# Performance work log

Hardware: AMD Instinct MI355X
Metric: run time of the kernel (lower is better)

## Reference

```python
import jax, jax.numpy as jnp
import numpy as np

B, S, D, H = 2, 2048, 2048, 16
HD = D // H
RESIDUAL_SCALE = 1.0
EPS = 1e-6


def setup_inputs() -> dict:
    key = jax.random.key(0)
    ks = jax.random.split(key, 6)
    x = jax.random.normal(ks[0], (B, S, D), jnp.float32)
    # rotary tables: emb = cat(freqs, freqs), shape [S, HD]
    inv_freq = 1.0 / (10000.0 ** (jnp.arange(0, HD, 2, dtype=jnp.float32) / HD))
    t = jnp.arange(S, dtype=jnp.float32)
    freqs = jnp.einsum('s,f->sf', t, inv_freq)
    emb = jnp.concatenate([freqs, freqs], axis=-1)
    cos, sin = jnp.cos(emb), jnp.sin(emb)
    sc = 0.02
    w_qkv = jax.random.normal(ks[1], (3 * D, D), jnp.float32) * sc
    w_out = jax.random.normal(ks[2], (D, D), jnp.float32) * sc
    w_fc1 = jax.random.normal(ks[3], (4 * D, D), jnp.float32) * sc
    w_fc2 = jax.random.normal(ks[4], (D, 4 * D), jnp.float32) * sc
    g1 = jnp.ones((D,), jnp.float32)
    g2 = jnp.ones((D,), jnp.float32)
    return {'x': x, 'cos': cos, 'sin': sin, 'g1': g1, 'g2': g2,
            'w_qkv': w_qkv, 'w_out': w_out, 'w_fc1': w_fc1, 'w_fc2': w_fc2}


def _rmsnorm(x, g):
    xf = x.astype(jnp.float32)
    norm = jnp.sqrt(jnp.mean(xf * xf, axis=-1, keepdims=True) + EPS)
    return g * (xf / norm)


def _rotate_half(x):
    x1, x2 = jnp.split(x, 2, axis=-1)
    return jnp.concatenate([-x2, x1], axis=-1)


def _rope(t, cos, sin):
    # t: [B, S, H, HD]; cos/sin: [S, HD]
    c = cos[None, :, None, :]
    s = sin[None, :, None, :]
    return t * c + _rotate_half(t) * s


def reference(x, cos, sin, g1, g2, w_qkv, w_out, w_fc1, w_fc2):
    b, s, d = x.shape
    x_skip = x
    h = _rmsnorm(x, g1)
    qkv = (h @ w_qkv.T).reshape(b, s, 3, H, HD)
    q = _rope(qkv[:, :, 0], cos, sin)
    k = _rope(qkv[:, :, 1], cos, sin)
    v = qkv[:, :, 2]  # rotary is identity on v
    scale = 1.0 / jnp.sqrt(jnp.asarray(HD, dtype=q.dtype))
    scores = jnp.einsum('bqhd,bkhd->bhqk', q, k) * scale
    causal = jnp.triu(jnp.ones((s, s), dtype=bool), k=1)
    scores = jnp.where(causal[None, None], -jnp.inf, scores)
    attn = jax.nn.softmax(scores, axis=-1)
    o = jnp.einsum('bhqk,bkhd->bqhd', attn, v).reshape(b, s, d)
    x = x_skip + RESIDUAL_SCALE * (o @ w_out.T)
    x_skip = x
    h = _rmsnorm(x, g2)
    h = jax.nn.gelu(h @ w_fc1.T, approximate=True) @ w_fc2.T
    return x_skip + RESIDUAL_SCALE * h
```

## Files before the change

kernel.cpp:

```cpp
#include <hip/hip_runtime.h>
#include <stdint.h>

typedef unsigned short u16;
typedef u16 u16x4 __attribute__((ext_vector_type(4)));
typedef u16 u16x8 __attribute__((ext_vector_type(8)));
typedef __bf16 bf16x8 __attribute__((ext_vector_type(8)));
typedef float f32x4 __attribute__((ext_vector_type(4)));
typedef float f32x16 __attribute__((ext_vector_type(16)));

#define MFMA16 __builtin_amdgcn_mfma_f32_16x16x32_bf16
#define MFMA32 __builtin_amdgcn_mfma_f32_32x32x16_bf16

static __device__ __forceinline__ float b2f(u16 u) {
    union { unsigned int i; float f; } v; v.i = ((unsigned int)u) << 16; return v.f;
}
static __device__ __forceinline__ u16 f2b(float f) {
    union { float f; unsigned int i; } v; v.f = f;
    unsigned int r = (v.i + 0x7fffu + ((v.i >> 16) & 1u)) >> 16;
    return (u16)r;
}
static __device__ __forceinline__ unsigned pk2(float lo, float hi) {
    union { __bf16 b[2]; unsigned u; } t;
    t.b[0] = (__bf16)lo; t.b[1] = (__bf16)hi; return t.u;
}
static __device__ __forceinline__ void gload_lds16(const void* g, void* l) {
    __builtin_amdgcn_global_load_lds((__attribute__((address_space(1))) void*)g,
                                     (__attribute__((address_space(3))) void*)l,
                                     16, 0, 0);
}

__global__ __launch_bounds__(256) void cvt_k(const float* __restrict__ in,
                                             u16* __restrict__ out, long n) {
    long i = ((long)blockIdx.x * 256 + threadIdx.x) * 4;
    if (i >= n) return;
    float4 v = *(const float4*)(in + i);
    u16x4 o; o[0] = f2b(v.x); o[1] = f2b(v.y); o[2] = f2b(v.z); o[3] = f2b(v.w);
    *(u16x4*)(out + i) = o;
}

__global__ __launch_bounds__(256) void addred_k(float* __restrict__ xout,
                                                const float* __restrict__ p0,
                                                const float* __restrict__ p1) {
    long i = ((long)blockIdx.x * 256 + threadIdx.x) * 4;
    float4 a = *(const float4*)(xout + i);
    float4 b = *(const float4*)(p0 + i);
    float4 c = *(const float4*)(p1 + i);
    a.x += b.x + c.x; a.y += b.y + c.y; a.z += b.z + c.z; a.w += b.w + c.w;
    *(float4*)(xout + i) = a;
}

__global__ __launch_bounds__(256) void addrednorm_k(float* __restrict__ xout,
                                                    const float* __restrict__ x,
                                                    const float* __restrict__ p0,
                                                    const float* __restrict__ p1,
                                                    const float* __restrict__ g,
                                                    u16* __restrict__ out) {
    const long row = blockIdx.x;
    const int tid = threadIdx.x;
    const long base = row * 2048;
    float4 a = *(const float4*)(x + base + tid * 4);
    float4 b = *(const float4*)(p0 + base + tid * 4);
    float4 c = *(const float4*)(p1 + base + tid * 4);
    a.x += b.x + c.x; a.y += b.y + c.y; a.z += b.z + c.z; a.w += b.w + c.w;
    float4 a2 = *(const float4*)(x + base + 1024 + tid * 4);
    float4 b2 = *(const float4*)(p0 + base + 1024 + tid * 4);
    float4 c2 = *(const float4*)(p1 + base + 1024 + tid * 4);
    a2.x += b2.x + c2.x; a2.y += b2.y + c2.y;
    a2.z += b2.z + c2.z; a2.w += b2.w + c2.w;
    *(float4*)(xout + base + tid * 4) = a;
    *(float4*)(xout + base + 1024 + tid * 4) = a2;
    float ss = a.x*a.x + a.y*a.y + a.z*a.z + a.w*a.w
             + a2.x*a2.x + a2.y*a2.y + a2.z*a2.z + a2.w*a2.w;
    #pragma unroll
    for (int d = 1; d < 64; d <<= 1) ss += __shfl_xor(ss, d);
    __shared__ float red[4];
    if ((tid & 63) == 0) red[tid >> 6] = ss;
    __syncthreads();
    float tot = red[0] + red[1] + red[2] + red[3];
    float rinv = rsqrtf(tot * (1.0f / 2048.0f) + 1e-6f);
    float4 g0 = *(const float4*)(g + tid * 4);
    float4 g1 = *(const float4*)(g + 1024 + tid * 4);
    u16x4 o0, o1;
    o0[0] = f2b(a.x * g0.x * rinv); o0[1] = f2b(a.y * g0.y * rinv);
    o0[2] = f2b(a.z * g0.z * rinv); o0[3] = f2b(a.w * g0.w * rinv);
    o1[0] = f2b(a2.x * g1.x * rinv); o1[1] = f2b(a2.y * g1.y * rinv);
    o1[2] = f2b(a2.z * g1.z * rinv); o1[3] = f2b(a2.w * g1.w * rinv);
    *(u16x4*)(out + base + tid * 4) = o0;
    *(u16x4*)(out + base + 1024 + tid * 4) = o1;
}

__global__ __launch_bounds__(256) void rmsnorm_k(const float* __restrict__ x,
                                                 const float* __restrict__ g,
                                                 u16* __restrict__ out) {
    const long row = blockIdx.x;
    const int tid = threadIdx.x;
    const float* xr = x + row * 2048;
    float4 a = *(const float4*)(xr + tid * 4);
    float4 b = *(const float4*)(xr + 1024 + tid * 4);
    float ss = a.x*a.x + a.y*a.y + a.z*a.z + a.w*a.w
             + b.x*b.x + b.y*b.y + b.z*b.z + b.w*b.w;
    #pragma unroll
    for (int d = 1; d < 64; d <<= 1) ss += __shfl_xor(ss, d);
    __shared__ float red[4];
    if ((tid & 63) == 0) red[tid >> 6] = ss;
    __syncthreads();
    float tot = red[0] + red[1] + red[2] + red[3];
    float rinv = rsqrtf(tot * (1.0f / 2048.0f) + 1e-6f);
    float4 g0 = *(const float4*)(g + tid * 4);
    float4 g1 = *(const float4*)(g + 1024 + tid * 4);
    u16x4 o0, o1;
    o0[0] = f2b(a.x * g0.x * rinv); o0[1] = f2b(a.y * g0.y * rinv);
    o0[2] = f2b(a.z * g0.z * rinv); o0[3] = f2b(a.w * g0.w * rinv);
    o1[0] = f2b(b.x * g1.x * rinv); o1[1] = f2b(b.y * g1.y * rinv);
    o1[2] = f2b(b.z * g1.z * rinv); o1[3] = f2b(b.w * g1.w * rinv);
    *(u16x4*)(out + row * 2048 + tid * 4) = o0;
    *(u16x4*)(out + row * 2048 + 1024 + tid * 4) = o1;
}

__global__ __launch_bounds__(256) void rope_k(u16* __restrict__ qkv,
                                              const float* __restrict__ cosb,
                                              const float* __restrict__ sinb) {
    long idx = (long)blockIdx.x * 256 + threadIdx.x;
    int d = (int)(idx & 15) * 4;
    int h = (int)((idx >> 4) & 15);
    int which = (int)((idx >> 8) & 1);
    long row = idx >> 9;
    int s = (int)(row & 2047);
    u16* base = qkv + row * 6144 + which * 2048 + h * 128;
    u16x4 ua = *(u16x4*)(base + d);
    u16x4 ub = *(u16x4*)(base + d + 64);
    float4 c4 = *(const float4*)(cosb + (long)s * 128 + d);
    float4 s4 = *(const float4*)(sinb + (long)s * 128 + d);
    float cc[4] = {c4.x, c4.y, c4.z, c4.w};
    float sn[4] = {s4.x, s4.y, s4.z, s4.w};
    float scale = (which == 0) ? 0.08838834764831845f : 1.0f;
    u16x4 oa, ob;
    #pragma unroll
    for (int j = 0; j < 4; ++j) {
        float a = b2f(ua[j]), b = b2f(ub[j]);
        oa[j] = f2b((a * cc[j] - b * sn[j]) * scale);
        ob[j] = f2b((b * cc[j] + a * sn[j]) * scale);
    }
    *(u16x4*)(base + d) = oa;
    *(u16x4*)(base + d + 64) = ob;
}

__global__ __launch_bounds__(256) void vtrans_k(const u16* __restrict__ qkv,
                                                u16* __restrict__ vt) {
    __shared__ u16 t[128 * 65];
    const int bh = blockIdx.y, b = bh >> 4, h = bh & 15;
    const int s0 = blockIdx.x * 64;
    const int tid = threadIdx.x;
    #pragma unroll
    for (int it = 0; it < 4; ++it) {
        int flat = it * 256 + tid;
        int sl = flat >> 4, slot = flat & 15;
        u16x8 v = *(const u16x8*)(qkv + (long)(b * 2048 + s0 + sl) * 6144 + 4096 +
                                  h * 128 + slot * 8);
        #pragma unroll
        for (int j = 0; j < 8; ++j) t[(slot * 8 + j) * 65 + sl] = v[j];
    }
    __syncthreads();
    #pragma unroll
    for (int it = 0; it < 4; ++it) {
        int flat = it * 256 + tid;
        int d = flat >> 3, sg = flat & 7;
        u16x8 v;
        #pragma unroll
        for (int j = 0; j < 8; ++j) v[j] = t[d * 65 + sg * 8 + j];
        *(u16x8*)(vt + ((long)bh * 128 + d) * 2048 + s0 + sg * 8) = v;
    }
}

#define DS_A(BUF, SM, KK) (*(const bf16x8*)(ldsb + (BUF)*32768 + \
        ((((SM)*2) + (KK)) << 10) + rin64 + cst2))
#define DS_B(BUF, SN, KK) (*(const bf16x8*)(ldsb + 65536 + (BUF)*32768 + \
        ((((SN)*2) + (KK)) << 10) + rin64 + cst2))
#define STAGE_A(BUF, SK, KT) do { \
    gload_lds16(sA0 + ((long)(KT)*64 + (SK)*32), ldsb + (BUF)*32768 + (w4 + (SK))*1024); \
    gload_lds16(sA1 + ((long)(KT)*64 + (SK)*32), ldsb + (BUF)*32768 + (w4 + 2 + (SK))*1024); \
} while (0)
#define STAGE_B(BUF, SK, KT) do { \
    gload_lds16(sB0 + ((long)(KT)*64 + (SK)*32), ldsb + 65536 + (BUF)*32768 + (w4 + (SK))*1024); \
    gload_lds16(sB1 + ((long)(KT)*64 + (SK)*32), ldsb + 65536 + (BUF)*32768 + (w4 + 2 + (SK))*1024); \
} while (0)
#define PHASE(BUF, MH, KK, RDB, STAGE_STMT, VM) do { \
    bf16x8 af[4]; \
    _Pragma("unroll") \
    for (int m = 0; m < 4; ++m) af[m] = DS_A(BUF, wr8 + (MH)*4 + m, KK); \
    if (RDB) { \
        bfr[0] = DS_B(BUF, wc4 + 0, KK); bfr[1] = DS_B(BUF, wc4 + 1, KK); \
        bfr[2] = DS_B(BUF, wc4 + 2, KK); bfr[3] = DS_B(BUF, wc4 + 3, KK); \
    } \
    STAGE_STMT; \
    if (VM) { asm volatile("s_waitcnt vmcnt(6)" ::: "memory"); } \
    __builtin_amdgcn_sched_barrier(0); \
    __builtin_amdgcn_s_barrier(); \
    __builtin_amdgcn_sched_barrier(0); \
    __builtin_amdgcn_s_setprio(1); \
    _Pragma("unroll") \
    for (int m = 0; m < 4; ++m) \
        _Pragma("unroll") \
        for (int n = 0; n < 4; ++n) \
            acc[(MH)*4 + m][n] = MFMA16(af[m], bfr[n], acc[(MH)*4 + m][n], 0, 0, 0); \
    __builtin_amdgcn_s_setprio(0); \
    __builtin_amdgcn_sched_barrier(0); \
    __builtin_amdgcn_s_barrier(); \
    __builtin_amdgcn_sched_barrier(0); \
} while (0)

template <int EPI>
__global__ __launch_bounds__(512, 2) void gemm256(const u16* __restrict__ A,
                                                  const u16* __restrict__ W,
                                                  int M, int N, int K,
                                                  u16* outb, float* outf,
                                                  const float* res, int ksplit) {
    __shared__ u16 lds_[65536];
    char* ldsb = (char*)lds_;
    const int tid = threadIdx.x;
    const int w = tid >> 6, l = tid & 63;
    const int w4 = w * 4;
    const int wr8 = (w >> 2) * 8;
    const int wc4 = (w & 3) * 4;
    const int rin64 = (l & 15) * 64;
    const int cst2 = ((((l >> 4) * 8) ^ (((l >> 3) & 1) << 4)) << 1);

    const int nbn = N >> 8;
    const int nbm = M >> 8;
    const int nwg = gridDim.x;
    const int cpx = nwg >> 3;
    const int bid = blockIdx.x;
    int wg = (bid & 7) * cpx + (bid >> 3);
    int kseg = 0;
    int Keff = K;
    if (ksplit == 2) {
        kseg = wg & 1;
        wg >>= 1;
        Keff = K >> 1;
    }
    const int grp = 8 * nbn;
    const int g8 = wg / grp;
    const int rem = wg - g8 * grp;
    const int bm0 = g8 * 8;
    const int gmh = (nbm - bm0 < 8) ? (nbm - bm0) : 8;
    const int bn = rem / gmh;
    const int bm = bm0 + rem % gmh;
    const u16* Ab = A + (long)kseg * Keff;
    const u16* Wb = W + (long)kseg * Keff;

    const int r4 = l >> 2;
    const int clog = ((l & 3) * 8) ^ (((r4 >> 3) & 1) << 4);
    const u16* sA0 = Ab + ((long)bm * 256 + (w * 2 + 0) * 16 + r4) * K + clog;
    const u16* sA1 = Ab + ((long)bm * 256 + (w * 2 + 1) * 16 + r4) * K + clog;
    const u16* sB0 = Wb + ((long)bn * 256 + (w * 2 + 0) * 16 + r4) * K + clog;
    const u16* sB1 = Wb + ((long)bn * 256 + (w * 2 + 1) * 16 + r4) * K + clog;

    f32x4 acc[8][4];
    #pragma unroll
    for (int m = 0; m < 8; ++m)
        #pragma unroll
        for (int n = 0; n < 4; ++n) acc[m][n] = (f32x4){0.f, 0.f, 0.f, 0.f};
    bf16x8 bfr[4];

    const int nkt = Keff >> 6;
    const int niter = nkt >> 1;

    STAGE_B(0, 0, 0); STAGE_A(0, 0, 0); STAGE_B(0, 1, 0); STAGE_A(0, 1, 0);
    STAGE_B(1, 0, 1); STAGE_A(1, 0, 1); STAGE_B(1, 1, 1);
    asm volatile("s_waitcnt vmcnt(6)" ::: "memory");
    __builtin_amdgcn_sched_barrier(0);
    __builtin_amdgcn_s_barrier();
    __builtin_amdgcn_sched_barrier(0);

    for (int it = 0; it < niter; ++it) {
        const int t = it * 2;
        const int t1 = t + 1;
        const int t2 = (t + 2 < nkt) ? t + 2 : nkt - 1;
        const int t3 = (t + 3 < nkt) ? t + 3 : nkt - 1;
        PHASE(0, 0, 0, 1, STAGE_A(1, 1, t1), 0);
        PHASE(0, 1, 0, 0, STAGE_B(0, 0, t2), 0);
        PHASE(0, 0, 1, 1, STAGE_A(0, 0, t2), 0);
        PHASE(0, 1, 1, 0, STAGE_B(0, 1, t2), 1);
        PHASE(1, 0, 0, 1, STAGE_A(0, 1, t2), 0);
        PHASE(1, 1, 0, 0, STAGE_B(1, 0, t3), 0);
        PHASE(1, 0, 1, 1, STAGE_A(1, 0, t3), 0);
        PHASE(1, 1, 1, 0, STAGE_B(1, 1, t3), 1);
    }
    asm volatile("s_waitcnt vmcnt(0)" ::: "memory");

    const int rb = bm * 256 + (wr8 >> 3) * 128 + ((l >> 4) << 2);
    const int cb = bn * 256 + (w & 3) * 64 + (l & 15);
    float* pf = (EPI == 3) ? (outf + (long)kseg * M * N) : outf;
    #pragma unroll
    for (int m = 0; m < 8; ++m) {
        #pragma unroll
        for (int r = 0; r < 4; ++r) {
            long row = rb + m * 16 + r;
            #pragma unroll
            for (int n = 0; n < 4; ++n) {
                long col = cb + n * 16;
                float v = acc[m][n][r];
                if (EPI == 1) {
                    pf[row * N + col] = res[row * N + col] + v;
                } else if (EPI == 2) {
                    float u = 0.7978845608028654f * v * (1.0f + 0.044715f * v * v);
                    float e = __expf(2.0f * u);
                    float tgl = 1.0f - 2.0f / (e + 1.0f);
                    outb[row * N + col] = f2b(0.5f * v * (1.0f + tgl));
                } else if (EPI == 3) {
                    pf[row * N + col] = v;
                } else {
                    outb[row * N + col] = f2b(v);
                }
            }
        }
    }
}

struct AttnState {
    f32x16 acc[4];
    float m_i, l_i;
};

template <bool DIAG>
static __device__ __forceinline__ void attn_tile(
    int kv0, int qg, bool do_g1, int l31, int hi,
    const u16* __restrict__ Ks, const u16* __restrict__ Vt,
    const bf16x8 (&qf)[8], AttnState& st)
{
    f32x16 sacc0, sacc1;
    #pragma unroll
    for (int r = 0; r < 16; ++r) { sacc0[r] = 0.f; sacc1[r] = 0.f; }

    #pragma unroll
    for (int dsl = 0; dsl < 8; ++dsl) {
        int slot = dsl * 2 + hi;
        int kv = l31;
        int sw = (slot & 8) | ((slot & 7) ^ (kv & 7));
        bf16x8 kf = *(const bf16x8*)(Ks + kv * 128 + sw * 8);
        sacc0 = MFMA32(kf, qf[dsl], sacc0, 0, 0, 0);
    }
    if (do_g1) {
        #pragma unroll
        for (int dsl = 0; dsl < 8; ++dsl) {
            int slot = dsl * 2 + hi;
            int kv = 32 + l31;
            int sw = (slot & 8) | ((slot & 7) ^ (kv & 7));
            bf16x8 kf = *(const bf16x8*)(Ks + kv * 128 + sw * 8);
            sacc1 = MFMA32(kf, qf[dsl], sacc1, 0, 0, 0);
        }
    }

    float sv[2][16];
    #pragma unroll
    for (int r = 0; r < 16; ++r) {
        sv[0][r] = sacc0[r];
        sv[1][r] = do_g1 ? sacc1[r] : -INFINITY;
    }
    if (DIAG) {
        #pragma unroll
        for (int g = 0; g < 2; ++g)
            #pragma unroll
            for (int r = 0; r < 16; ++r) {
                int kvg = kv0 + g * 32 + ((r & 3) + 8 * (r >> 2) + 4 * hi);
                if (kvg > qg) sv[g][r] = -INFINITY;
            }
    }

    float mx = sv[0][0];
    #pragma unroll
    for (int r = 1; r < 16; ++r) mx = fmaxf(mx, sv[0][r]);
    #pragma unroll
    for (int r = 0; r < 16; ++r) mx = fmaxf(mx, sv[1][r]);
    mx = fmaxf(mx, __shfl_xor(mx, 32));

    bool defer = __all(mx <= st.m_i + 8.0f);
    if (!defer) {
        float mnew = fmaxf(st.m_i, mx);
        float f = __expf(st.m_i - mnew);
        st.l_i *= f;
        #pragma unroll
        for (int dblk = 0; dblk < 4; ++dblk)
            #pragma unroll
            for (int r = 0; r < 16; ++r) st.acc[dblk][r] *= f;
        st.m_i = mnew;
    }

    float ssum = 0.f;
    #pragma unroll
    for (int g = 0; g < 2; ++g)
        #pragma unroll
        for (int r = 0; r < 16; ++r) {
            float e = __expf(sv[g][r] - st.m_i);
            sv[g][r] = e;
            ssum += e;
        }
    ssum += __shfl_xor(ssum, 32);
    st.l_i += ssum;

    unsigned w[2][4][2];
    #pragma unroll
    for (int g = 0; g < 2; ++g)
        #pragma unroll
        for (int q4 = 0; q4 < 4; ++q4) {
            w[g][q4][0] = pk2(sv[g][4 * q4 + 0], sv[g][4 * q4 + 1]);
            w[g][q4][1] = pk2(sv[g][4 * q4 + 2], sv[g][4 * q4 + 3]);
        }
    bf16x8 pfrag[4];
    #pragma unroll
    for (int ks = 0; ks < 4; ++ks) {
        int g = ks >> 1, h2 = ks & 1;
        unsigned o0 = hi ? w[g][2 * h2 + 1][0] : w[g][2 * h2][0];
        unsigned o1 = hi ? w[g][2 * h2 + 1][1] : w[g][2 * h2][1];
        unsigned t0 = hi ? w[g][2 * h2][0] : w[g][2 * h2 + 1][0];
        unsigned t1 = hi ? w[g][2 * h2][1] : w[g][2 * h2 + 1][1];
        unsigned s0v = __shfl_xor(t0, 32);
        unsigned s1v = __shfl_xor(t1, 32);
        union { unsigned u[4]; bf16x8 v; } cv;
        cv.u[0] = hi ? s0v : o0;
        cv.u[1] = hi ? s1v : o1;
        cv.u[2] = hi ? o0 : s0v;
        cv.u[3] = hi ? o1 : s1v;
        pfrag[ks] = cv.v;
    }

    #pragma unroll
    for (int dblk = 0; dblk < 4; ++dblk) {
        int d = dblk * 32 + l31;
        #pragma unroll
        for (int ks = 0; ks < 4; ++ks) {
            if (ks >= 2 && !do_g1) continue;
            int slot = ks * 2 + hi;
            bf16x8 vf = *(const bf16x8*)(Vt + d * 64 + (slot ^ (d & 7)) * 8);
            st.acc[dblk] = MFMA32(vf, pfrag[ks], st.acc[dblk], 0, 0, 0);
        }
    }
}

__global__ __launch_bounds__(256) void attn3_k(const u16* __restrict__ qkv,
                                               const u16* __restrict__ vt,
                                               u16* __restrict__ out) {
    const int bh = blockIdx.y;
    const int b = bh >> 4, h = bh & 15;
    const int qb = blockIdx.x;
    const int q0 = qb * 128;
    const int tid = threadIdx.x, wave = tid >> 6, lane = tid & 63;
    const int l31 = lane & 31, hi = lane >> 5;
    const int brow = b * 2048;
    __shared__ u16 Ks_lds[2][64 * 128];
    __shared__ u16 Vt_lds[2][128 * 64];

    const int krow = tid >> 4;
    const int kslot = tid & 15;
    const int vrow = tid >> 3;
    const int vslot = tid & 7;

    bf16x8 qf[8];
    {
        const u16* qp = qkv + (long)(brow + q0 + wave * 32 + l31) * 6144 +
                        h * 128 + hi * 8;
        #pragma unroll
        for (int dsl = 0; dsl < 8; ++dsl) qf[dsl] = *(const bf16x8*)(qp + dsl * 16);
    }

    AttnState st;
    st.m_i = -INFINITY; st.l_i = 0.f;
    #pragma unroll
    for (int dblk = 0; dblk < 4; ++dblk)
        #pragma unroll
        for (int r = 0; r < 16; ++r) st.acc[dblk][r] = 0.f;

    const int r0 = q0 + wave * 32;
    const int qg = r0 + l31;
    const int nt = 2 * qb + 2;
    int cur = 0;

#define STAGE_KV(BUF, KV0) do { \
    _Pragma("unroll") \
    for (int i = 0; i < 4; ++i) { \
        int kv = i * 16 + krow; \
        int sw = (kslot & 8) | ((kslot & 7) ^ (kv & 7)); \
        const u16* src = qkv + (long)(brow + (KV0) + kv) * 6144 + 2048 + \
                         h * 128 + sw * 8; \
        gload_lds16(src, (char*)Ks_lds[BUF] + (i * 16 + wave * 4) * 256); \
    } \
    _Pragma("unroll") \
    for (int i = 0; i < 4; ++i) { \
        int d = i * 32 + vrow; \
        int sw = vslot ^ (d & 7); \
        const u16* src = vt + ((long)bh * 128 + d) * 2048 + (KV0) + sw * 8; \
        gload_lds16(src, (char*)Vt_lds[BUF] + (i * 32 + wave * 8) * 128); \
    } \
} while (0)

    STAGE_KV(0, 0);
    for (int t = 0; t < nt; ++t) {
        const int kv0 = t * 64;
        const bool more = (t + 1 < nt);
        if (more) {
            if (cur) STAGE_KV(0, kv0 + 64); else STAGE_KV(1, kv0 + 64);
        }
        if (more) { asm volatile("s_waitcnt vmcnt(8)" ::: "memory"); }
        else      { asm volatile("s_waitcnt vmcnt(0)" ::: "memory"); }
        __builtin_amdgcn_sched_barrier(0);
        __builtin_amdgcn_s_barrier();
        __builtin_amdgcn_sched_barrier(0);
        {
            const u16* Ks = Ks_lds[cur];
            const u16* Vt_ = Vt_lds[cur];
            const int delta = r0 - kv0;
            if (delta >= 64)
                attn_tile<false>(kv0, qg, true, l31, hi, Ks, Vt_, qf, st);
            else if (delta >= 0)
                attn_tile<true>(kv0, qg, delta >= 32, l31, hi, Ks, Vt_, qf, st);
        }
        __builtin_amdgcn_sched_barrier(0);
        __builtin_amdgcn_s_barrier();
        __builtin_amdgcn_sched_barrier(0);
        cur ^= 1;
    }
#undef STAGE_KV

    float inv = 1.0f / st.l_i;
    long orow = (long)(brow + q0 + wave * 32 + l31);
    #pragma unroll
    for (int dblk = 0; dblk < 4; ++dblk)
        #pragma unroll
        for (int rq = 0; rq < 4; ++rq) {
            u16x4 o4;
            #pragma unroll
            for (int m = 0; m < 4; ++m) o4[m] = f2b(st.acc[dblk][rq * 4 + m] * inv);
            int d = dblk * 32 + 8 * rq + 4 * hi;
            *(u16x4*)(out + orow * 2048 + h * 128 + d) = o4;
        }
}

extern "C" void kernel_launch(void* const* d_in, const int* in_sizes, int n_in,
                              void* d_out, int out_size, void* d_ws, size_t ws_size,
                              hipStream_t stream) {
    const float* x     = (const float*)d_in[0];
    const float* cosb  = (const float*)d_in[1];
    const float* sinb  = (const float*)d_in[2];
    const float* g1    = (const float*)d_in[3];
    const float* g2    = (const float*)d_in[4];
    const float* w_qkv = (const float*)d_in[5];
    const float* w_out = (const float*)d_in[6];
    const float* w_fc1 = (const float*)d_in[7];
    const float* w_fc2 = (const float*)d_in[8];

    char* ws = (char*)d_ws;
    u16* wqkv_b = (u16*)(ws);
    u16* wout_b = (u16*)(ws + 25165824);
    u16* wfc1_b = (u16*)(ws + 33554432);
    u16* wfc2_b = (u16*)(ws + 67108864);
    u16* h_b    = (u16*)(ws + 100663296);
    u16* qkv_b  = (u16*)(ws + 117440512);
    u16* attn_b = (u16*)(ws + 167772160);
    u16* vt_b   = h_b;
    u16* hg_b   = qkv_b;
    float* part = (float*)ws;
    float* pop  = (float*)(ws + 100663296);
    float* xout = (float*)d_out;

    cvt_k<<<12288, 256, 0, stream>>>(w_qkv, wqkv_b, 12582912L);
    cvt_k<<<4096, 256, 0, stream>>>(w_out, wout_b, 4194304L);
    cvt_k<<<16384, 256, 0, stream>>>(w_fc1, wfc1_b, 16777216L);
    cvt_k<<<16384, 256, 0, stream>>>(w_fc2, wfc2_b, 16777216L);

    rmsnorm_k<<<4096, 256, 0, stream>>>(x, g1, h_b);
    gemm256<0><<<384, 512, 0, stream>>>(h_b, wqkv_b, 4096, 6144, 2048,
                                        qkv_b, nullptr, nullptr, 1);
    rope_k<<<8192, 256, 0, stream>>>(qkv_b, cosb, sinb);
    vtrans_k<<<dim3(32, 32), 256, 0, stream>>>(qkv_b, vt_b);
    attn3_k<<<dim3(16, 32), 256, 0, stream>>>(qkv_b, vt_b, attn_b);
    gemm256<3><<<256, 512, 0, stream>>>(attn_b, wout_b, 4096, 2048, 2048,
                                        nullptr, pop, nullptr, 2);
    addrednorm_k<<<4096, 256, 0, stream>>>(xout, x, pop, pop + 8388608, g2, h_b);
    gemm256<2><<<512, 512, 0, stream>>>(h_b, wfc1_b, 4096, 8192, 2048,
                                        hg_b, nullptr, nullptr, 1);
    gemm256<3><<<256, 512, 0, stream>>>(hg_b, wfc2_b, 4096, 2048, 8192,
                                        nullptr, part, nullptr, 2);
    addred_k<<<8192, 256, 0, stream>>>(xout, part, part + 8388608);
}
```

Measured before the change: 604.7 us.

## Fuse V transpose into QKV GEMM epilogue and merge A/B staging

The QKV projection GEMM gets a new epilogue that writes the V columns directly in transposed [b,h,d,s] layout into the output buffer. This removes the separate vtrans kernel and its extra read and write of V. The GEMM main loop now issues A and B tile loads together in every other phase rather than alternating them, with the vmcnt wait adjusted to match. Workspace aliasing is also rearranged so the out-projection partial sums land in d_out and the qkv region, which drops __restrict__ on addrednorm because its output now aliases an input. The V epilogue writes short strided u16x4 stores, and the staging change alters how memory loads overlap with the MFMA work.

```diff
diff --git a/kernel.cpp b/kernel.cpp
--- a/kernel.cpp
+++ b/kernel.cpp
@@ -49,9 +49,9 @@
     *(float4*)(xout + i) = a;
 }
 
-__global__ __launch_bounds__(256) void addrednorm_k(float* __restrict__ xout,
+__global__ __launch_bounds__(256) void addrednorm_k(float* xout,
                                                     const float* __restrict__ x,
-                                                    const float* __restrict__ p0,
+                                                    const float* p0,
                                                     const float* __restrict__ p1,
                                                     const float* __restrict__ g,
                                                     u16* __restrict__ out) {
@@ -145,42 +145,13 @@
     *(u16x4*)(base + d + 64) = ob;
 }
 
-__global__ __launch_bounds__(256) void vtrans_k(const u16* __restrict__ qkv,
-                                                u16* __restrict__ vt) {
-    __shared__ u16 t[128 * 65];
-    const int bh = blockIdx.y, b = bh >> 4, h = bh & 15;
-    const int s0 = blockIdx.x * 64;
-    const int tid = threadIdx.x;
-    #pragma unroll
-    for (int it = 0; it < 4; ++it) {
-        int flat = it * 256 + tid;
-        int sl = flat >> 4, slot = flat & 15;
-        u16x8 v = *(const u16x8*)(qkv + (long)(b * 2048 + s0 + sl) * 6144 + 4096 +
-                                  h * 128 + slot * 8);
-        #pragma unroll
-        for (int j = 0; j < 8; ++j) t[(slot * 8 + j) * 65 + sl] = v[j];
-    }
-    __syncthreads();
-    #pragma unroll
-    for (int it = 0; it < 4; ++it) {
-        int flat = it * 256 + tid;
-        int d = flat >> 3, sg = flat & 7;
-        u16x8 v;
-        #pragma unroll
-        for (int j = 0; j < 8; ++j) v[j] = t[d * 65 + sg * 8 + j];
-        *(u16x8*)(vt + ((long)bh * 128 + d) * 2048 + s0 + sg * 8) = v;
-    }
-}
-
 #define DS_A(BUF, SM, KK) (*(const bf16x8*)(ldsb + (BUF)*32768 + \
         ((((SM)*2) + (KK)) << 10) + rin64 + cst2))
 #define DS_B(BUF, SN, KK) (*(const bf16x8*)(ldsb + 65536 + (BUF)*32768 + \
         ((((SN)*2) + (KK)) << 10) + rin64 + cst2))
-#define STAGE_A(BUF, SK, KT) do { \
+#define STAGE_AB(BUF, SK, KT) do { \
     gload_lds16(sA0 + ((long)(KT)*64 + (SK)*32), ldsb + (BUF)*32768 + (w4 + (SK))*1024); \
     gload_lds16(sA1 + ((long)(KT)*64 + (SK)*32), ldsb + (BUF)*32768 + (w4 + 2 + (SK))*1024); \
-} while (0)
-#define STAGE_B(BUF, SK, KT) do { \
     gload_lds16(sB0 + ((long)(KT)*64 + (SK)*32), ldsb + 65536 + (BUF)*32768 + (w4 + (SK))*1024); \
     gload_lds16(sB1 + ((long)(KT)*64 + (SK)*32), ldsb + 65536 + (BUF)*32768 + (w4 + 2 + (SK))*1024); \
 } while (0)
@@ -193,7 +164,7 @@
         bfr[2] = DS_B(BUF, wc4 + 2, KK); bfr[3] = DS_B(BUF, wc4 + 3, KK); \
     } \
     STAGE_STMT; \
-    if (VM) { asm volatile("s_waitcnt vmcnt(6)" ::: "memory"); } \
+    if (VM) { asm volatile("s_waitcnt vmcnt(8)" ::: "memory"); } \
     __builtin_amdgcn_sched_barrier(0); \
     __builtin_amdgcn_s_barrier(); \
     __builtin_amdgcn_sched_barrier(0); \
@@ -214,7 +185,8 @@
                                                   const u16* __restrict__ W,
                                                   int M, int N, int K,
                                                   u16* outb, float* outf,
-                                                  const float* res, int ksplit) {
+                                                  float* outf2, const float* res,
+                                                  u16* vtw, int ksplit) {
     __shared__ u16 lds_[65536];
     char* ldsb = (char*)lds_;
     const int tid = threadIdx.x;
@@ -265,9 +237,8 @@
     const int nkt = Keff >> 6;
     const int niter = nkt >> 1;
 
-    STAGE_B(0, 0, 0); STAGE_A(0, 0, 0); STAGE_B(0, 1, 0); STAGE_A(0, 1, 0);
-    STAGE_B(1, 0, 1); STAGE_A(1, 0, 1); STAGE_B(1, 1, 1);
-    asm volatile("s_waitcnt vmcnt(6)" ::: "memory");
+    STAGE_AB(0, 0, 0); STAGE_AB(0, 1, 0); STAGE_AB(1, 0, 1);
+    asm volatile("s_waitcnt vmcnt(8)" ::: "memory");
     __builtin_amdgcn_sched_barrier(0);
     __builtin_amdgcn_s_barrier();
     __builtin_amdgcn_sched_barrier(0);
@@ -277,20 +248,46 @@
         const int t1 = t + 1;
         const int t2 = (t + 2 < nkt) ? t + 2 : nkt - 1;
         const int t3 = (t + 3 < nkt) ? t + 3 : nkt - 1;
-        PHASE(0, 0, 0, 1, STAGE_A(1, 1, t1), 0);
-        PHASE(0, 1, 0, 0, STAGE_B(0, 0, t2), 0);
-        PHASE(0, 0, 1, 1, STAGE_A(0, 0, t2), 0);
-        PHASE(0, 1, 1, 0, STAGE_B(0, 1, t2), 1);
-        PHASE(1, 0, 0, 1, STAGE_A(0, 1, t2), 0);
-        PHASE(1, 1, 0, 0, STAGE_B(1, 0, t3), 0);
-        PHASE(1, 0, 1, 1, STAGE_A(1, 0, t3), 0);
-        PHASE(1, 1, 1, 0, STAGE_B(1, 1, t3), 1);
+        PHASE(0, 0, 0, 1, STAGE_AB(1, 1, t1), 0);
+        PHASE(0, 1, 0, 0, ;, 1);
+        PHASE(0, 0, 1, 1, STAGE_AB(0, 0, t2), 0);
+        PHASE(0, 1, 1, 0, ;, 1);
+        PHASE(1, 0, 0, 1, STAGE_AB(0, 1, t2), 0);
+        PHASE(1, 1, 0, 0, ;, 1);
+        PHASE(1, 0, 1, 1, STAGE_AB(1, 0, t3), 0);
+        PHASE(1, 1, 1, 0, ;, 1);
     }
     asm volatile("s_waitcnt vmcnt(0)" ::: "memory");
 
     const int rb = bm * 256 + (wr8 >> 3) * 128 + ((l >> 4) << 2);
     const int cb = bn * 256 + (w & 3) * 64 + (l & 15);
-    float* pf = (EPI == 3) ? (outf + (long)kseg * M * N) : outf;
+    if (EPI == 4) {
+        const bool vreg = (cb >= 4096);
+        #pragma unroll
+        for (int m = 0; m < 8; ++m) {
+            long row0 = rb + m * 16;
+            #pragma unroll
+            for (int n = 0; n < 4; ++n) {
+                long col = cb + n * 16;
+                if (vreg) {
+                    int d = (int)col & 127;
+                    int hh = ((int)col >> 7) - 32;
+                    long bh = (row0 >> 11) * 16 + hh;
+                    int s = (int)(row0 & 2047);
+                    u16x4 o4;
+                    #pragma unroll
+                    for (int r = 0; r < 4; ++r) o4[r] = f2b(acc[m][n][r]);
+                    *(u16x4*)(vtw + (bh * 128 + d) * 2048 + s) = o4;
+                } else {
+                    #pragma unroll
+                    for (int r = 0; r < 4; ++r)
+                        outb[(row0 + r) * N + col] = f2b(acc[m][n][r]);
+                }
+            }
+        }
+        return;
+    }
+    float* pf = (EPI == 3) ? (kseg ? outf2 : outf) : outf;
     #pragma unroll
     for (int m = 0; m < 8; ++m) {
         #pragma unroll
@@ -556,10 +553,11 @@
     u16* h_b    = (u16*)(ws + 100663296);
     u16* qkv_b  = (u16*)(ws + 117440512);
     u16* attn_b = (u16*)(ws + 167772160);
-    u16* vt_b   = h_b;
     u16* hg_b   = qkv_b;
+    u16* vt_b   = (u16*)d_out;
+    float* p0op = (float*)d_out;
+    float* p1op = (float*)(ws + 117440512);
     float* part = (float*)ws;
-    float* pop  = (float*)(ws + 100663296);
     float* xout = (float*)d_out;
 
     cvt_k<<<12288, 256, 0, stream>>>(w_qkv, wqkv_b, 12582912L);
@@ -568,17 +566,20 @@
     cvt_k<<<16384, 256, 0, stream>>>(w_fc2, wfc2_b, 16777216L);
 
     rmsnorm_k<<<4096, 256, 0, stream>>>(x, g1, h_b);
-    gemm256<0><<<384, 512, 0, stream>>>(h_b, wqkv_b, 4096, 6144, 2048,
-                                        qkv_b, nullptr, nullptr, 1);
+    gemm256<4><<<384, 512, 0, stream>>>(h_b, wqkv_b, 4096, 6144, 2048,
+                                        qkv_b, nullptr, nullptr, nullptr,
+                                        vt_b, 1);
     rope_k<<<8192, 256, 0, stream>>>(qkv_b, cosb, sinb);
-    vtrans_k<<<dim3(32, 32), 256, 0, stream>>>(qkv_b, vt_b);
     attn3_k<<<dim3(16, 32), 256, 0, stream>>>(qkv_b, vt_b, attn_b);
     gemm256<3><<<256, 512, 0, stream>>>(attn_b, wout_b, 4096, 2048, 2048,
-                                        nullptr, pop, nullptr, 2);
-    addrednorm_k<<<4096, 256, 0, stream>>>(xout, x, pop, pop + 8388608, g2, h_b);
+                                        nullptr, p0op, p1op, nullptr,
+                                        nullptr, 2);
+    addrednorm_k<<<4096, 256, 0, stream>>>(xout, x, p0op, p1op, g2, h_b);
     gemm256<2><<<512, 512, 0, stream>>>(h_b, wfc1_b, 4096, 8192, 2048,
-                                        hg_b, nullptr, nullptr, 1);
+                                        hg_b, nullptr, nullptr, nullptr,
+                                        nullptr, 1);
     gemm256<3><<<256, 512, 0, stream>>>(hg_b, wfc2_b, 4096, 2048, 8192,
-                                        nullptr, part, nullptr, 2);
+                                        nullptr, part, part + 8388608, nullptr,
+                                        nullptr, 2);
     addred_k<<<8192, 256, 0, stream>>>(xout, part, part + 8388608);
 }
```

New measurement: 618.0 us. 1.02x slower.
